# Kernel optimization log

Measured on AMD Instinct MI355X. Metric: run time of the kernel, lower is better.

## Reference

```python
import jax, jax.numpy as jnp
import numpy as np

EPS = 1e-6
K = 20
NEG_SLOPE = 0.2

def knn_idx(x, k):
    # x: (B, D, N) flattened vector features; returns (B, N, k) neighbor indices
    inner = -2.0 * jnp.einsum('bdn,bdm->bnm', x, x)
    xx = jnp.sum(x * x, axis=1)  # (B, N)
    pd = -xx[:, :, None] - inner - xx[:, None, :]  # negative squared distance
    _, idx = jax.lax.top_k(pd, k)
    return idx

def get_graph_feature(x, k):
    # x: (B, C, 3, N) -> (B, 2C, 3, N, k) edge features (nbr - ctr, ctr)
    B, C, _, N = x.shape
    idx = knn_idx(x.reshape(B, C * 3, N), k)           # (B, N, k)
    feat = jnp.transpose(x, (0, 3, 1, 2))              # (B, N, C, 3)
    nb = jax.vmap(lambda f, i: f[i])(feat, idx)        # (B, N, k, C, 3)
    ctr = jnp.broadcast_to(feat[:, :, None], nb.shape)
    out = jnp.concatenate([nb - ctr, ctr], axis=3)     # (B, N, k, 2C, 3)
    return jnp.transpose(out, (0, 3, 4, 1, 2))

def vn_batchnorm(x, gamma, beta):
    # x: (B, C, 3, ...); BatchNorm (training stats) applied to vector norms
    norm = jnp.linalg.norm(x, axis=2) + EPS            # (B, C, ...)
    axes = (0,) + tuple(range(2, norm.ndim))
    mu = jnp.mean(norm, axis=axes, keepdims=True)
    var = jnp.var(norm, axis=axes, keepdims=True)
    shape = (1, -1) + (1,) * (norm.ndim - 2)
    nbn = (norm - mu) / jnp.sqrt(var + 1e-5) * gamma.reshape(shape) + beta.reshape(shape)
    return x / norm[:, :, None] * nbn[:, :, None]

def vn_linear_leakyrelu(x, w_feat, w_dir, gamma, beta):
    # x: (B, Cin, 3, ...) -> (B, Cout, 3, ...)
    p = jnp.einsum('oc,bc...->bo...', w_feat, x)
    p = vn_batchnorm(p, gamma, beta)
    d = jnp.einsum('oc,bc...->bo...', w_dir, x)
    dot = jnp.sum(p * d, axis=2, keepdims=True)
    dsq = jnp.sum(d * d, axis=2, keepdims=True)
    proj = p - (dot / (dsq + EPS)) * d
    return NEG_SLOPE * p + (1.0 - NEG_SLOPE) * jnp.where(dot >= 0, p, proj)

def _forward(x, w1, d1, g1, b1, w2, d2, g2, b2, w3, d3, g3, b3, w4, d4, g4, b4, w5, d5, g5, b5):
    h = jnp.transpose(x, (0, 2, 1))[:, None]           # (B, 1, 3, N)
    h = vn_linear_leakyrelu(get_graph_feature(h, K), w1, d1, g1, b1)
    x1 = jnp.mean(h, axis=-1)                          # mean_pool over k: (B, 21, 3, N)
    h = vn_linear_leakyrelu(get_graph_feature(x1, K), w2, d2, g2, b2)
    x2 = jnp.mean(h, axis=-1)                          # (B, 21, 3, N)
    h = vn_linear_leakyrelu(get_graph_feature(x2, K), w3, d3, g3, b3)
    x3 = jnp.mean(h, axis=-1)                          # (B, 42, 3, N)
    h = vn_linear_leakyrelu(get_graph_feature(x3, K), w4, d4, g4, b4)
    x4 = jnp.mean(h, axis=-1)                          # (B, 85, 3, N)
    cat = jnp.concatenate([x1, x2, x3, x4], axis=1)    # (B, 169, 3, N)
    return vn_linear_leakyrelu(cat, w5, d5, g5, b5)    # (B, 341, 3, N)

def setup_inputs():
    key = jax.random.key(0)
    B, N = 8, 1024
    d = {"x": jax.random.normal(key, (B, N, 3), dtype=jnp.float32)}
    feat_shapes = {"1": (21, 2), "2": (21, 42), "3": (42, 42), "4": (85, 84), "5": (341, 169)}
    dir_out = {"1": 21, "2": 21, "3": 42, "4": 85, "5": 1}  # conv5 shares nonlinearity -> 1 dir channel
    for i, (name, (co, ci)) in enumerate(feat_shapes.items()):
        k1, k2 = jax.random.split(jax.random.fold_in(key, i + 1))
        s = 1.0 / np.sqrt(ci)
        d["w" + name] = jax.random.uniform(k1, (co, ci), minval=-s, maxval=s, dtype=jnp.float32)
        d["d" + name] = jax.random.uniform(k2, (dir_out[name], ci), minval=-s, maxval=s, dtype=jnp.float32)
        d["g" + name] = jnp.ones((co,), dtype=jnp.float32)
        d["b" + name] = jnp.zeros((co,), dtype=jnp.float32)
    return d

def reference(x, w1, d1, g1, b1, w2, d2, g2, b2, w3, d3, g3, b3, w4, d4, g4, b4, w5, d5, g5, b5):
    return _forward(x, w1, d1, g1, b1, w2, d2, g2, b2, w3, d3, g3, b3, w4, d4, g4, b4, w5, d5, g5, b5)
```

## Files before the change

kernel.cpp:

```cpp
#include <hip/hip_runtime.h>
#include <math.h>

#define KNN 20
#define NS 0.2f
#define EPSV 1e-6f
#define QT 4
#define OT 8
#define CROW 507
#define SSPLIT 8

struct F3 { float x, y, z; };

extern __shared__ __align__(16) float smem[];

__global__ void k_transpose(const float* __restrict__ x, float* __restrict__ xt,
                            float* __restrict__ xx, int B, int N) {
    int i = blockIdx.x * blockDim.x + threadIdx.x;
    if (i >= B * N) return;
    int b = i / N, n = i % N;
    const float* src = x + (size_t)(b * N + n) * 3;
    float* dst = xt + (size_t)b * 3 * N + n;
    float s0 = src[0], s1 = src[1], s2 = src[2];
    dst[0] = s0;
    dst[(size_t)N] = s1;
    dst[(size_t)2 * N] = s2;
    float s = 0.f;
    s += s0 * s0;
    s += s1 * s1;
    s += s2 * s2;
    xx[i] = s;
}

__global__ void k_knn(const float* __restrict__ X, const float* __restrict__ xx,
                      int* __restrict__ idx,
                      int N, int D, long batchStride, long sliceOff) {
    int b = blockIdx.y;
    int q0 = blockIdx.x * QT;
    int tid = threadIdx.x;
    int lane = tid & 63;
    int wave = tid >> 6;

    __shared__ __align__(16) float qf[128 * QT];
    __shared__ __align__(16) float pd[QT][1024];

    const float* Xb = X + (size_t)b * batchStride + sliceOff;
    const float* xxb = xx + (size_t)b * N;

    for (int t = tid; t < QT * D; t += 256) {
        int d = t >> 2, q = t & 3;
        qf[d * QT + q] = Xb[(size_t)d * N + (q0 + q)];
    }
    __syncthreads();

    float a0x = 0.f, a0y = 0.f, a0z = 0.f, a0w = 0.f;
    float a1x = 0.f, a1y = 0.f, a1z = 0.f, a1w = 0.f;
    float a2x = 0.f, a2y = 0.f, a2z = 0.f, a2w = 0.f;
    float a3x = 0.f, a3y = 0.f, a3z = 0.f, a3w = 0.f;

    const float* mbase = Xb + 4 * tid;
#pragma unroll 3
    for (int d = 0; d < D; ++d) {
        float4 xm = *(const float4*)(mbase + (size_t)d * N);
        float4 qv = *(const float4*)(qf + d * QT);
        a0x += qv.x * xm.x; a0y += qv.x * xm.y; a0z += qv.x * xm.z; a0w += qv.x * xm.w;
        a1x += qv.y * xm.x; a1y += qv.y * xm.y; a1z += qv.y * xm.z; a1w += qv.y * xm.w;
        a2x += qv.z * xm.x; a2y += qv.z * xm.y; a2z += qv.z * xm.z; a2w += qv.z * xm.w;
        a3x += qv.w * xm.x; a3y += qv.w * xm.y; a3z += qv.w * xm.z; a3w += qv.w * xm.w;
    }

    {
        float4 m2 = *(const float4*)(xxb + 4 * tid);
        float4 qn = *(const float4*)(xxb + q0);
        float4 v;
        v.x = 2.f * a0x - qn.x - m2.x; v.y = 2.f * a0y - qn.x - m2.y;
        v.z = 2.f * a0z - qn.x - m2.z; v.w = 2.f * a0w - qn.x - m2.w;
        *(float4*)&pd[0][4 * tid] = v;
        v.x = 2.f * a1x - qn.y - m2.x; v.y = 2.f * a1y - qn.y - m2.y;
        v.z = 2.f * a1z - qn.y - m2.z; v.w = 2.f * a1w - qn.y - m2.w;
        *(float4*)&pd[1][4 * tid] = v;
        v.x = 2.f * a2x - qn.z - m2.x; v.y = 2.f * a2y - qn.z - m2.y;
        v.z = 2.f * a2z - qn.z - m2.z; v.w = 2.f * a2w - qn.z - m2.w;
        *(float4*)&pd[2][4 * tid] = v;
        v.x = 2.f * a3x - qn.w - m2.x; v.y = 2.f * a3y - qn.w - m2.y;
        v.z = 2.f * a3z - qn.w - m2.z; v.w = 2.f * a3w - qn.w - m2.w;
        *(float4*)&pd[3][4 * tid] = v;
    }
    __syncthreads();

    unsigned long long key[16];
#pragma unroll
    for (int t = 0; t < 16; ++t) {
        unsigned u = __float_as_uint(pd[wave][t * 64 + lane]);
        u ^= (unsigned)((int)u >> 31) | 0x80000000u;
        unsigned lo = (unsigned)(1023 - t * 64) - (unsigned)lane;
        key[t] = ((unsigned long long)u << 32) | (unsigned long long)lo;
    }

#define CE(a, b)                                        \
    {                                                   \
        unsigned long long ka = key[a], kb = key[b];    \
        bool sw = ka < kb;                              \
        key[a] = sw ? kb : ka;                          \
        key[b] = sw ? ka : kb;                          \
    }
    CE(0,1) CE(2,3) CE(4,5) CE(6,7) CE(8,9) CE(10,11) CE(12,13) CE(14,15)
    CE(0,2) CE(1,3) CE(4,6) CE(5,7) CE(8,10) CE(9,11) CE(12,14) CE(13,15)
    CE(1,2) CE(5,6) CE(9,10) CE(13,14)
    CE(0,4) CE(1,5) CE(2,6) CE(3,7) CE(8,12) CE(9,13) CE(10,14) CE(11,15)
    CE(2,4) CE(3,5) CE(10,12) CE(11,13)
    CE(1,2) CE(3,4) CE(5,6) CE(9,10) CE(11,12) CE(13,14)
    CE(0,8) CE(1,9) CE(2,10) CE(3,11) CE(4,12) CE(5,13) CE(6,14) CE(7,15)
    CE(4,8) CE(5,9) CE(6,10) CE(7,11)
    CE(2,4) CE(3,5) CE(6,8) CE(7,9) CE(10,12) CE(11,13)
    CE(1,2) CE(3,4) CE(5,6) CE(7,8) CE(9,10) CE(11,12) CE(13,14)
#undef CE

    __syncthreads();
    unsigned long long* kl = (unsigned long long*)&pd[wave][0];
#pragma unroll
    for (int t = 8; t < 16; ++t) kl[(t - 8) * 64 + lane] = key[t];
    int nspill = 0;

    long outBase = ((long)b * N + q0 + wave) * KNN;
    for (int it = 0; it < KNN; ++it) {
        unsigned long long bk = key[0];
#pragma unroll
        for (int off = 32; off >= 1; off >>= 1) {
            unsigned long long ok = __shfl_xor(bk, off, 64);
            if (ok > bk) bk = ok;
        }
        int bi = 1023 - (int)(bk & 1023u);
        if (lane == 0) idx[outBase + it] = bi;
        if ((bi & 63) == lane) {
            key[0] = key[1]; key[1] = key[2]; key[2] = key[3]; key[3] = key[4];
            key[4] = key[5]; key[5] = key[6]; key[6] = key[7];
            int sidx = nspill < 8 ? nspill : 7;
            unsigned long long nv = kl[sidx * 64 + lane];
            key[7] = (nspill < 8) ? nv : 0ull;
            nspill++;
        }
    }
}

__global__ void k_matmul_pair_lds(const float* __restrict__ X, const float* __restrict__ W,
                                  const float* __restrict__ Dw,
                                  float* __restrict__ U, float* __restrict__ V,
                                  float* __restrict__ UD, float* __restrict__ VD,
                                  int C, int Co, int CoP, int TILE,
                                  int rowStride, int colOff) {
    const int CP = C * CoP;
    float* wts = smem;
    float* xs = smem + 4 * CP;

    int tid = threadIdx.x;
    int bn0 = blockIdx.x * TILE;
    int C3 = C * 3;

    int npad = CoP - Co;
    if (npad) {
        for (int t = tid; t < 4 * C * npad; t += 256) {
            int q = t / npad, oo = Co + t % npad;
            int mat = q / C, c = q % C;
            wts[mat * CP + c * CoP + oo] = 0.f;
        }
    }
    int twoCC = 2 * C * Co;
    for (int t = tid; t < twoCC; t += 256) {
        int o = t / (2 * C), c = t % (2 * C);
        float w = W[t], dw = Dw[t];
        if (c < C) {
            wts[c * CoP + o] = w;
            wts[2 * CP + c * CoP + o] = dw;
        } else {
            wts[CP + (c - C) * CoP + o] = w;
            wts[3 * CP + (c - C) * CoP + o] = dw;
        }
    }
    for (int t = tid; t < TILE * C3; t += 256) {
        int p = t / C3, cc = t % C3;
        xs[t] = X[(size_t)(bn0 + p) * rowStride + colOff + cc];
    }
    __syncthreads();
    for (int t = tid; t < CP; t += 256) {
        wts[CP + t] -= wts[t];
        wts[3 * CP + t] -= wts[2 * CP + t];
    }
    __syncthreads();

    int GPP = CoP >> 2;
    int items = TILE * GPP;
    for (int e = tid; e < items; e += 256) {
        int p = e / GPP, og = e - p * GPP;
        int o0 = og * 4;
        const float* xr = xs + p * C3;

        float aU[4][3], aV[4][3], aDu[4][3], aDv[4][3];
#pragma unroll
        for (int i = 0; i < 4; ++i)
#pragma unroll
            for (int j = 0; j < 3; ++j) {
                aU[i][j] = 0.f; aV[i][j] = 0.f; aDu[i][j] = 0.f; aDv[i][j] = 0.f;
            }

        for (int c = 0; c < C; ++c) {
            float x0 = xr[c * 3], x1 = xr[c * 3 + 1], x2 = xr[c * 3 + 2];
            const float* wp = wts + c * CoP + o0;
            float4 wa4 = *(const float4*)(wp);
            float4 wb4 = *(const float4*)(wp + CP);
            float4 da4 = *(const float4*)(wp + 2 * CP);
            float4 db4 = *(const float4*)(wp + 3 * CP);
            float wav[4] = {wa4.x, wa4.y, wa4.z, wa4.w};
            float wbv[4] = {wb4.x, wb4.y, wb4.z, wb4.w};
            float dav[4] = {da4.x, da4.y, da4.z, da4.w};
            float dbv[4] = {db4.x, db4.y, db4.z, db4.w};
#pragma unroll
            for (int i = 0; i < 4; ++i) {
                aU[i][0] += wav[i] * x0; aU[i][1] += wav[i] * x1; aU[i][2] += wav[i] * x2;
                aV[i][0] += wbv[i] * x0; aV[i][1] += wbv[i] * x1; aV[i][2] += wbv[i] * x2;
                aDu[i][0] += dav[i] * x0; aDu[i][1] += dav[i] * x1; aDu[i][2] += dav[i] * x2;
                aDv[i][0] += dbv[i] * x0; aDv[i][1] += dbv[i] * x1; aDv[i][2] += dbv[i] * x2;
            }
        }

        size_t base = ((size_t)(bn0 + p) * Co + o0) * 3;
#pragma unroll
        for (int i = 0; i < 4; ++i) {
            int o = o0 + i;
            if (o < Co) {
                size_t off = base + (size_t)i * 3;
                U[off] = aU[i][0]; U[off + 1] = aU[i][1]; U[off + 2] = aU[i][2];
                V[off] = aV[i][0]; V[off + 1] = aV[i][1]; V[off + 2] = aV[i][2];
                UD[off] = aDu[i][0]; UD[off + 1] = aDu[i][1]; UD[off + 2] = aDu[i][2];
                VD[off] = aDv[i][0]; VD[off + 1] = aDv[i][1]; VD[off + 2] = aDv[i][2];
            }
        }
    }
}

__global__ void k_stats_edge_det(const float* __restrict__ U, const float* __restrict__ V,
                                 const int* __restrict__ idx, float* __restrict__ partials,
                                 int N, int Co, int BN) {
    int o = blockIdx.x;
    int s = blockIdx.y;
    int tid = threadIdx.x;
    int P = BN / SSPLIT;
    int g0 = s * P;

    __shared__ float Ush[3072];
    __shared__ float r1[256], r2[256];

    for (int t = tid; t < P; t += 256) {
        F3 u3 = *(const F3*)(U + ((size_t)(g0 + t) * Co + o) * 3);
        Ush[t * 3 + 0] = u3.x;
        Ush[t * 3 + 1] = u3.y;
        Ush[t * 3 + 2] = u3.z;
    }
    __syncthreads();

    float s1 = 0.f, s2 = 0.f;
    for (int pl = tid; pl < P; pl += 256) {
        int g = g0 + pl;
        F3 v3 = *(const F3*)(V + ((size_t)g * Co + o) * 3);
        float v0 = v3.x, v1 = v3.y, v2 = v3.z;
        const int* ip = idx + (size_t)g * KNN;
        for (int kk = 0; kk < KNN; ++kk) {
            const float* Ur = Ush + ip[kk] * 3;
            float p0 = Ur[0] + v0;
            float p1 = Ur[1] + v1;
            float p2 = Ur[2] + v2;
            float nm = sqrtf(p0 * p0 + p1 * p1 + p2 * p2) + EPSV;
            s1 += nm;
            s2 += nm * nm;
        }
    }
    r1[tid] = s1; r2[tid] = s2;
    __syncthreads();
    for (int st = 128; st > 0; st >>= 1) {
        if (tid < st) { r1[tid] += r1[tid + st]; r2[tid] += r2[tid + st]; }
        __syncthreads();
    }
    if (tid == 0) {
        partials[(o * SSPLIT + s) * 2] = r1[0];
        partials[(o * SSPLIT + s) * 2 + 1] = r2[0];
    }
}

__global__ void k_final_edge_p(const float* __restrict__ U, const float* __restrict__ V,
                               const float* __restrict__ UD, const float* __restrict__ VD,
                               const int* __restrict__ idx, const float* __restrict__ partials,
                               const float* __restrict__ gamma, const float* __restrict__ beta,
                               float* __restrict__ catp,
                               int N, int Co, int colOff, float cnt, int total) {
    int g = blockIdx.x * 256 + threadIdx.x;
    if (g >= total) return;
    int o = g % Co;
    int r = g / Co;
    int n = r % N;
    int b = r / N;

    float s1 = 0.f, s2 = 0.f;
    for (int s = 0; s < SSPLIT; ++s) {
        s1 += partials[(o * SSPLIT + s) * 2];
        s2 += partials[(o * SSPLIT + s) * 2 + 1];
    }
    float mu = s1 / cnt;
    float var = s2 / cnt - mu * mu;
    float inv = rsqrtf(var + 1e-5f);
    float gmm = gamma[o], bt = beta[o];

    size_t ctr = ((size_t)(b * N + n) * Co + o) * 3;
    F3 vc = *(const F3*)(V + ctr);
    F3 wc = *(const F3*)(VD + ctr);
    float v0 = vc.x, v1 = vc.y, v2 = vc.z;
    float w0 = wc.x, w1 = wc.y, w2 = wc.z;
    const int* ip = idx + ((size_t)b * N + n) * KNN;

    float a0 = 0.f, a1 = 0.f, a2 = 0.f;
    for (int kk = 0; kk < KNN; ++kk) {
        int m = ip[kk];
        size_t nb = ((size_t)(b * N + m) * Co + o) * 3;
        F3 un = *(const F3*)(U + nb);
        F3 dn = *(const F3*)(UD + nb);
        float p0 = un.x + v0;
        float p1 = un.y + v1;
        float p2 = un.z + v2;
        float nm = sqrtf(p0 * p0 + p1 * p1 + p2 * p2) + EPSV;
        float nbn = (nm - mu) * inv * gmm + bt;
        float sc = nbn / nm;
        p0 *= sc; p1 *= sc; p2 *= sc;
        float d0 = dn.x + w0;
        float d1 = dn.y + w1;
        float d2 = dn.z + w2;
        float dot = p0 * d0 + p1 * d1 + p2 * d2;
        if (dot >= 0.f) {
            a0 += p0; a1 += p1; a2 += p2;
        } else {
            float f = dot / (d0 * d0 + d1 * d1 + d2 * d2 + EPSV);
            a0 += NS * p0 + (1.f - NS) * (p0 - f * d0);
            a1 += NS * p1 + (1.f - NS) * (p1 - f * d1);
            a2 += NS * p2 + (1.f - NS) * (p2 - f * d2);
        }
    }
    const float invk = 1.f / (float)KNN;
    float* outp = catp + (size_t)(b * N + n) * CROW + colOff + o * 3;
    outp[0] = a0 * invk;
    outp[1] = a1 * invk;
    outp[2] = a2 * invk;
}

__global__ void k_transpose_cat(const float* __restrict__ catp, float* __restrict__ catn,
                                int N, int c0, int CC,
                                float* __restrict__ xx, int doSq) {
    int ytiles = (CC + 31) >> 5;
    if (doSq && (int)blockIdx.y == ytiles) {
        if (blockIdx.z != 0) return;
        int i = blockIdx.x * 256 + threadIdx.x;
        const float* row = catp + (size_t)i * CROW + c0;
        float s = 0.f;
        for (int c = 0; c < CC; ++c) {
            float v = row[c];
            s += v * v;
        }
        xx[i] = s;
        return;
    }

    __shared__ float tile[32][33];
    int b = blockIdx.z;
    int n0 = blockIdx.x * 32;
    int cb = blockIdx.y * 32;
    int tid = threadIdx.x;
    int tx = tid & 31, ty = tid >> 5;

#pragma unroll
    for (int rr = 0; rr < 4; ++rr) {
        int nl = ty + rr * 8;
        int c = cb + tx;
        if (c < CC)
            tile[nl][tx] = catp[(size_t)(b * N + n0 + nl) * CROW + c0 + c];
    }
    __syncthreads();
#pragma unroll
    for (int rr = 0; rr < 4; ++rr) {
        int cl = ty + rr * 8;
        int c = cb + cl;
        if (c < CC)
            catn[(size_t)b * CROW * N + (size_t)(c0 + c) * N + n0 + tx] = tile[tx][cl];
    }
}

__global__ void k_matmul_plain(const float* __restrict__ X, const float* __restrict__ W,
                               const float* __restrict__ Dw,
                               float* __restrict__ U, float* __restrict__ Ud,
                               int N, int Cin, int Cout, long batchStride, long sliceOff) {
    int ot = blockIdx.y;
    int b = blockIdx.z;
    int tid = threadIdx.x;
    int n = blockIdx.x * 512 + 2 * tid;

    const float* Wp; float* Up; int CoutE; int o0;
    if (ot == (int)gridDim.y - 1) {
        Wp = Dw; Up = Ud; CoutE = 1; o0 = 0;
    } else {
        Wp = W; Up = U; CoutE = Cout; o0 = ot * OT;
    }

    __shared__ __align__(16) float wsm[OT][176];
    for (int t = tid; t < OT * Cin; t += 256) {
        int oo = t / Cin, c = t % Cin;
        int o = o0 + oo;
        wsm[oo][c] = (o < CoutE) ? Wp[(size_t)o * Cin + c] : 0.f;
    }
    __syncthreads();

    const float* Xp = X + (size_t)b * batchStride + sliceOff + n;
    float au[OT][3][2];
#pragma unroll
    for (int oo = 0; oo < OT; ++oo)
#pragma unroll
        for (int j = 0; j < 3; ++j) {
            au[oo][j][0] = 0.f; au[oo][j][1] = 0.f;
        }

    int c = 0;
    for (; c + 4 <= Cin; c += 4) {
        float2 xv[4][3];
#pragma unroll
        for (int cc = 0; cc < 4; ++cc)
#pragma unroll
            for (int j = 0; j < 3; ++j)
                xv[cc][j] = *(const float2*)(Xp + ((size_t)(c + cc) * 3 + j) * N);
#pragma unroll
        for (int oo = 0; oo < OT; ++oo) {
            float4 w4 = *(const float4*)&wsm[oo][c];
            float wv[4] = {w4.x, w4.y, w4.z, w4.w};
#pragma unroll
            for (int j = 0; j < 3; ++j) {
#pragma unroll
                for (int cc = 0; cc < 4; ++cc) {
                    au[oo][j][0] += wv[cc] * xv[cc][j].x;
                    au[oo][j][1] += wv[cc] * xv[cc][j].y;
                }
            }
        }
    }
    for (; c < Cin; ++c) {
        float2 xv[3];
#pragma unroll
        for (int j = 0; j < 3; ++j)
            xv[j] = *(const float2*)(Xp + ((size_t)c * 3 + j) * N);
#pragma unroll
        for (int oo = 0; oo < OT; ++oo) {
            float wv = wsm[oo][c];
#pragma unroll
            for (int j = 0; j < 3; ++j) {
                au[oo][j][0] += wv * xv[j].x;
                au[oo][j][1] += wv * xv[j].y;
            }
        }
    }
#pragma unroll
    for (int oo = 0; oo < OT; ++oo) {
        int o = o0 + oo;
        if (o < CoutE) {
#pragma unroll
            for (int j = 0; j < 3; ++j) {
                float2 st; st.x = au[oo][j][0]; st.y = au[oo][j][1];
                *(float2*)&Up[(((size_t)b * CoutE + o) * 3 + j) * N + n] = st;
            }
        }
    }
}

__global__ void k_stats_plain_det(const float* __restrict__ U, float* __restrict__ mv,
                                  int N, int Cout, int BN, float cnt) {
    int o = blockIdx.x;
    int tid = threadIdx.x;
    float s1 = 0.f, s2 = 0.f;
    for (int g = tid; g < BN; g += 256) {
        int b = g / N, n = g % N;
        const float* Ub = U + (((size_t)b * Cout + o) * 3) * N;
        float p0 = Ub[n], p1 = Ub[(size_t)N + n], p2 = Ub[(size_t)2 * N + n];
        float nm = sqrtf(p0 * p0 + p1 * p1 + p2 * p2) + EPSV;
        s1 += nm;
        s2 += nm * nm;
    }
    __shared__ float r1[256], r2[256];
    r1[tid] = s1; r2[tid] = s2;
    __syncthreads();
    for (int st = 128; st > 0; st >>= 1) {
        if (tid < st) { r1[tid] += r1[tid + st]; r2[tid] += r2[tid + st]; }
        __syncthreads();
    }
    if (tid == 0) {
        float mu = r1[0] / cnt;
        float var = r2[0] / cnt - mu * mu;
        mv[2 * o] = mu;
        mv[2 * o + 1] = rsqrtf(var + 1e-5f);
    }
}

__global__ void k_final_plain(const float* __restrict__ U, const float* __restrict__ Dv,
                              const float* __restrict__ mv,
                              const float* __restrict__ gamma, const float* __restrict__ beta,
                              float* __restrict__ out, int N, int Cout) {
    int b = blockIdx.z, o = blockIdx.y, tid = threadIdx.x;
    int n = blockIdx.x * 256 + tid;
    float mu = mv[2 * o];
    float inv = mv[2 * o + 1];
    float g = gamma[o], bt = beta[o];

    const float* Ub = U + (((size_t)b * Cout + o) * 3) * N;
    float p0 = Ub[n], p1 = Ub[(size_t)N + n], p2 = Ub[(size_t)2 * N + n];
    float nm = sqrtf(p0 * p0 + p1 * p1 + p2 * p2) + EPSV;
    float nbn = (nm - mu) * inv * g + bt;
    float sc = nbn / nm;
    p0 *= sc; p1 *= sc; p2 *= sc;

    float d0 = Dv[((size_t)b * 3 + 0) * N + n];
    float d1 = Dv[((size_t)b * 3 + 1) * N + n];
    float d2 = Dv[((size_t)b * 3 + 2) * N + n];
    float dot = p0 * d0 + p1 * d1 + p2 * d2;
    float o0, o1, o2;
    if (dot >= 0.f) {
        o0 = p0; o1 = p1; o2 = p2;
    } else {
        float f = dot / (d0 * d0 + d1 * d1 + d2 * d2 + EPSV);
        o0 = NS * p0 + (1.f - NS) * (p0 - f * d0);
        o1 = NS * p1 + (1.f - NS) * (p1 - f * d1);
        o2 = NS * p2 + (1.f - NS) * (p2 - f * d2);
    }
    size_t ob = (((size_t)b * Cout + o) * 3) * N + n;
    out[ob] = o0;
    out[ob + (size_t)N] = o1;
    out[ob + (size_t)2 * N] = o2;
}

extern "C" void kernel_launch(void* const* d_in, const int* in_sizes, int n_in,
                              void* d_out, int out_size, void* d_ws, size_t ws_size,
                              hipStream_t stream) {
    (void)in_sizes; (void)n_in; (void)out_size; (void)ws_size;
    const int B = 8, N = 1024;

    const float* x = (const float*)d_in[0];
    const float* W[5]; const float* Dw[5]; const float* G[5]; const float* Bt[5];
    for (int l = 0; l < 5; ++l) {
        W[l]  = (const float*)d_in[1 + 4 * l];
        Dw[l] = (const float*)d_in[2 + 4 * l];
        G[l]  = (const float*)d_in[3 + 4 * l];
        Bt[l] = (const float*)d_in[4 + 4 * l];
    }

    float* ws = (float*)d_ws;
    size_t off = 0;
    float* xt = ws + off;     off += (size_t)B * 3 * N;
    int* idx = (int*)(ws + off); off += (size_t)B * N * KNN;
    float* catp = ws + off;   off += (size_t)B * N * CROW;
    float* catn = ws + off;   off += (size_t)B * N * CROW;
    float* Up = ws + off;     off += (size_t)B * N * 85 * 3;
    float* Vp = ws + off;     off += (size_t)B * N * 85 * 3;
    float* UDp = ws + off;    off += (size_t)B * N * 85 * 3;
    float* VDp = ws + off;    off += (size_t)B * N * 85 * 3;
    float* U5 = ws + off;     off += (size_t)B * 341 * 3 * N;
    float* d5buf = ws + off;  off += (size_t)B * 3 * N;
    float* xx = ws + off;     off += (size_t)B * N;
    float* partials = ws + off; off += (size_t)341 * SSPLIT * 2;
    float* mv = ws + off;     off += 2 * 341;

    k_transpose<<<(B * N + 255) / 256, 256, 0, stream>>>(x, xt, xx, B, N);

    const int Cin_[4]  = {1, 21, 21, 42};
    const int Cout_[4] = {21, 21, 42, 85};
    const int inOff_[4] = {-1, 0, 21, 42};
    const int outOff_[4] = {0, 21, 42, 84};
    const int Tile_[4] = {32, 32, 32, 8};

    const int BN = B * N;

    for (int l = 0; l < 4; ++l) {
        int C = Cin_[l], Co = Cout_[l];
        int D = C * 3;
        int CoP = (Co + 3) & ~3;
        int TILE = Tile_[l];

        const float* Xn; long bs, so;
        if (inOff_[l] < 0) { Xn = xt; bs = (long)3 * N; so = 0; }
        else { Xn = catn; bs = (long)CROW * N; so = (long)inOff_[l] * 3 * N; }

        const float* Xp; int rs, co;
        if (inOff_[l] < 0) { Xp = x; rs = 3; co = 0; }
        else { Xp = catp; rs = CROW; co = inOff_[l] * 3; }

        dim3 gk(N / QT, B);
        k_knn<<<gk, 256, 0, stream>>>(Xn, xx, idx, N, D, bs, so);

        size_t smemB = (size_t)(4 * C * CoP + TILE * C * 3) * sizeof(float);
        k_matmul_pair_lds<<<(B * N) / TILE, 256, smemB, stream>>>(
            Xp, W[l], Dw[l], Up, Vp, UDp, VDp, C, Co, CoP, TILE, rs, co);

        dim3 gst(Co, SSPLIT);
        k_stats_edge_det<<<gst, 256, 0, stream>>>(Up, Vp, idx, partials, N, Co, BN);

        int total = BN * Co;
        k_final_edge_p<<<(total + 255) / 256, 256, 0, stream>>>(
            Up, Vp, UDp, VDp, idx, partials, G[l], Bt[l], catp,
            N, Co, outOff_[l] * 3, (float)((size_t)BN * KNN), total);

        int CC = Co * 3;
        int doSq = (l < 3) ? 1 : 0;
        dim3 gt(N / 32, (CC + 31) / 32 + doSq, B);
        k_transpose_cat<<<gt, 256, 0, stream>>>(catp, catn, N, outOff_[l] * 3, CC, xx, doSq);
    }

    {
        long bs = (long)CROW * N, so = 0;
        dim3 gm5(N / 512, (341 + OT - 1) / OT + 1, B);
        k_matmul_plain<<<gm5, 256, 0, stream>>>(catn, W[4], Dw[4], U5, d5buf,
                                                N, 169, 341, bs, so);
        k_stats_plain_det<<<341, 256, 0, stream>>>(U5, mv, N, 341, BN, (float)BN);
        dim3 gs5(N / 256, 341, B);
        k_final_plain<<<gs5, 256, 0, stream>>>(U5, d5buf, mv, G[4], Bt[4],
                                               (float*)d_out, N, 341);
    }
}
```

Measured before the change: 719.8 us.

## Fuse edge final stage with cat transpose and squared-norm computation

Merges the per-edge normalization/leaky-ReLU/mean-pool kernel with the following transpose and row squared-norm kernel. Each block handles TN points for all output channels, stages the results in shared memory, then writes both row-major and channel-major copies and computes xx for the next kNN. This removes one launch and a global round trip through catp, and it hoists the BN statistics reduction into shared memory once per block. The cost is that each block has only TN*Co items, so parallelism drops for small Co, and the channel-major stores are only TN-contiguous (8 floats), which makes them poorly coalesced.

Measured after the change: 676.7 us. 6.0% less time.

```diff
diff --git a/kernel.cpp b/kernel.cpp
--- a/kernel.cpp
+++ b/kernel.cpp
@@ -6,6 +6,7 @@
 #define EPSV 1e-6f
 #define QT 4
 #define OT 8
+#define TN 8
 #define CROW 507
 #define SSPLIT 8
 
@@ -285,107 +286,97 @@
     }
 }
 
-__global__ void k_final_edge_p(const float* __restrict__ U, const float* __restrict__ V,
-                               const float* __restrict__ UD, const float* __restrict__ VD,
-                               const int* __restrict__ idx, const float* __restrict__ partials,
-                               const float* __restrict__ gamma, const float* __restrict__ beta,
-                               float* __restrict__ catp,
-                               int N, int Co, int colOff, float cnt, int total) {
-    int g = blockIdx.x * 256 + threadIdx.x;
-    if (g >= total) return;
-    int o = g % Co;
-    int r = g / Co;
-    int n = r % N;
-    int b = r / N;
-
-    float s1 = 0.f, s2 = 0.f;
-    for (int s = 0; s < SSPLIT; ++s) {
-        s1 += partials[(o * SSPLIT + s) * 2];
-        s2 += partials[(o * SSPLIT + s) * 2 + 1];
-    }
-    float mu = s1 / cnt;
-    float var = s2 / cnt - mu * mu;
-    float inv = rsqrtf(var + 1e-5f);
-    float gmm = gamma[o], bt = beta[o];
-
-    size_t ctr = ((size_t)(b * N + n) * Co + o) * 3;
-    F3 vc = *(const F3*)(V + ctr);
-    F3 wc = *(const F3*)(VD + ctr);
-    float v0 = vc.x, v1 = vc.y, v2 = vc.z;
-    float w0 = wc.x, w1 = wc.y, w2 = wc.z;
-    const int* ip = idx + ((size_t)b * N + n) * KNN;
-
-    float a0 = 0.f, a1 = 0.f, a2 = 0.f;
-    for (int kk = 0; kk < KNN; ++kk) {
-        int m = ip[kk];
-        size_t nb = ((size_t)(b * N + m) * Co + o) * 3;
-        F3 un = *(const F3*)(U + nb);
-        F3 dn = *(const F3*)(UD + nb);
-        float p0 = un.x + v0;
-        float p1 = un.y + v1;
-        float p2 = un.z + v2;
-        float nm = sqrtf(p0 * p0 + p1 * p1 + p2 * p2) + EPSV;
-        float nbn = (nm - mu) * inv * gmm + bt;
-        float sc = nbn / nm;
-        p0 *= sc; p1 *= sc; p2 *= sc;
-        float d0 = dn.x + w0;
-        float d1 = dn.y + w1;
-        float d2 = dn.z + w2;
-        float dot = p0 * d0 + p1 * d1 + p2 * d2;
-        if (dot >= 0.f) {
-            a0 += p0; a1 += p1; a2 += p2;
-        } else {
-            float f = dot / (d0 * d0 + d1 * d1 + d2 * d2 + EPSV);
-            a0 += NS * p0 + (1.f - NS) * (p0 - f * d0);
-            a1 += NS * p1 + (1.f - NS) * (p1 - f * d1);
-            a2 += NS * p2 + (1.f - NS) * (p2 - f * d2);
-        }
-    }
+__global__ void k_final_fused(const float* __restrict__ U, const float* __restrict__ V,
+                              const float* __restrict__ UD, const float* __restrict__ VD,
+                              const int* __restrict__ idx, const float* __restrict__ partials,
+                              const float* __restrict__ gamma, const float* __restrict__ beta,
+                              float* __restrict__ catp, float* __restrict__ catn,
+                              float* __restrict__ xx,
+                              int N, int Co, int colOff, float cnt, int doSq) {
+    int b = blockIdx.y;
+    int n0 = blockIdx.x * TN;
+    int tid = threadIdx.x;
+    int CC = Co * 3;
+
+    __shared__ float tile[TN * 255];
+    __shared__ float muS[85], invS[85];
+
+    for (int o = tid; o < Co; o += 256) {
+        float s1 = 0.f, s2 = 0.f;
+        for (int s = 0; s < SSPLIT; ++s) {
+            s1 += partials[(o * SSPLIT + s) * 2];
+            s2 += partials[(o * SSPLIT + s) * 2 + 1];
+        }
+        float mu = s1 / cnt;
+        float var = s2 / cnt - mu * mu;
+        muS[o] = mu;
+        invS[o] = rsqrtf(var + 1e-5f);
+    }
+    __syncthreads();
+
     const float invk = 1.f / (float)KNN;
-    float* outp = catp + (size_t)(b * N + n) * CROW + colOff + o * 3;
-    outp[0] = a0 * invk;
-    outp[1] = a1 * invk;
-    outp[2] = a2 * invk;
-}
-
-__global__ void k_transpose_cat(const float* __restrict__ catp, float* __restrict__ catn,
-                                int N, int c0, int CC,
-                                float* __restrict__ xx, int doSq) {
-    int ytiles = (CC + 31) >> 5;
-    if (doSq && (int)blockIdx.y == ytiles) {
-        if (blockIdx.z != 0) return;
-        int i = blockIdx.x * 256 + threadIdx.x;
-        const float* row = catp + (size_t)i * CROW + c0;
+    int items = TN * Co;
+    for (int e = tid; e < items; e += 256) {
+        int nl = e / Co, o = e - nl * Co;
+        int n = n0 + nl;
+        float mu = muS[o], inv = invS[o];
+        float gmm = gamma[o], bt = beta[o];
+
+        size_t ctr = ((size_t)(b * N + n) * Co + o) * 3;
+        F3 vc = *(const F3*)(V + ctr);
+        F3 wc = *(const F3*)(VD + ctr);
+        float v0 = vc.x, v1 = vc.y, v2 = vc.z;
+        float w0 = wc.x, w1 = wc.y, w2 = wc.z;
+        const int* ip = idx + ((size_t)b * N + n) * KNN;
+
+        float a0 = 0.f, a1 = 0.f, a2 = 0.f;
+        for (int kk = 0; kk < KNN; ++kk) {
+            int m = ip[kk];
+            size_t nb = ((size_t)(b * N + m) * Co + o) * 3;
+            F3 un = *(const F3*)(U + nb);
+            F3 dn = *(const F3*)(UD + nb);
+            float p0 = un.x + v0;
+            float p1 = un.y + v1;
+            float p2 = un.z + v2;
+            float nm = sqrtf(p0 * p0 + p1 * p1 + p2 * p2) + EPSV;
+            float nbn = (nm - mu) * inv * gmm + bt;
+            float sc = nbn / nm;
+            p0 *= sc; p1 *= sc; p2 *= sc;
+            float d0 = dn.x + w0;
+            float d1 = dn.y + w1;
+            float d2 = dn.z + w2;
+            float dot = p0 * d0 + p1 * d1 + p2 * d2;
+            if (dot >= 0.f) {
+                a0 += p0; a1 += p1; a2 += p2;
+            } else {
+                float f = dot / (d0 * d0 + d1 * d1 + d2 * d2 + EPSV);
+                a0 += NS * p0 + (1.f - NS) * (p0 - f * d0);
+                a1 += NS * p1 + (1.f - NS) * (p1 - f * d1);
+                a2 += NS * p2 + (1.f - NS) * (p2 - f * d2);
+            }
+        }
+        tile[nl * CC + o * 3 + 0] = a0 * invk;
+        tile[nl * CC + o * 3 + 1] = a1 * invk;
+        tile[nl * CC + o * 3 + 2] = a2 * invk;
+    }
+    __syncthreads();
+
+    for (int t = tid; t < TN * CC; t += 256) {
+        int nl = t / CC, c = t - nl * CC;
+        catp[(size_t)(b * N + n0 + nl) * CROW + colOff + c] = tile[nl * CC + c];
+    }
+    for (int t = tid; t < TN * CC; t += 256) {
+        int c = t >> 3, nl = t & (TN - 1);
+        catn[(size_t)b * CROW * N + (size_t)(colOff + c) * N + n0 + nl] = tile[nl * CC + c];
+    }
+    if (doSq && tid < TN) {
+        const float* row = tile + tid * CC;
         float s = 0.f;
         for (int c = 0; c < CC; ++c) {
             float v = row[c];
             s += v * v;
         }
-        xx[i] = s;
-        return;
-    }
-
-    __shared__ float tile[32][33];
-    int b = blockIdx.z;
-    int n0 = blockIdx.x * 32;
-    int cb = blockIdx.y * 32;
-    int tid = threadIdx.x;
-    int tx = tid & 31, ty = tid >> 5;
-
-#pragma unroll
-    for (int rr = 0; rr < 4; ++rr) {
-        int nl = ty + rr * 8;
-        int c = cb + tx;
-        if (c < CC)
-            tile[nl][tx] = catp[(size_t)(b * N + n0 + nl) * CROW + c0 + c];
-    }
-    __syncthreads();
-#pragma unroll
-    for (int rr = 0; rr < 4; ++rr) {
-        int cl = ty + rr * 8;
-        int c = cb + cl;
-        if (c < CC)
-            catn[(size_t)b * CROW * N + (size_t)(c0 + c) * N + n0 + tx] = tile[tx][cl];
+        xx[(size_t)b * N + n0 + tid] = s;
     }
 }
 
@@ -601,15 +592,12 @@
         dim3 gst(Co, SSPLIT);
         k_stats_edge_det<<<gst, 256, 0, stream>>>(Up, Vp, idx, partials, N, Co, BN);
 
-        int total = BN * Co;
-        k_final_edge_p<<<(total + 255) / 256, 256, 0, stream>>>(
-            Up, Vp, UDp, VDp, idx, partials, G[l], Bt[l], catp,
-            N, Co, outOff_[l] * 3, (float)((size_t)BN * KNN), total);
-
-        int CC = Co * 3;
         int doSq = (l < 3) ? 1 : 0;
-        dim3 gt(N / 32, (CC + 31) / 32 + doSq, B);
-        k_transpose_cat<<<gt, 256, 0, stream>>>(catp, catn, N, outOff_[l] * 3, CC, xx, doSq);
+        dim3 gf(N / TN, B);
+        k_final_fused<<<gf, 256, 0, stream>>>(
+            Up, Vp, UDp, VDp, idx, partials, G[l], Bt[l],
+            catp, catn, xx, N, Co, outOff_[l] * 3,
+            (float)((size_t)BN * KNN), doSq);
     }
 
     {
```
